# Performance work log

Measured on AMD Instinct MI355X. Metric: run time of the kernel, lower is better.

The kernel has to match this reference:

```python
import jax, jax.numpy as jnp
import numpy as np

M_POS = 0.5
M_NEG_SIM = 0.1
LAM_NEG = 1.0


def setup_inputs() -> dict:
    key = jax.random.key(0)
    N, d, G = 8192, 1024, 64
    codebook = jax.random.normal(key, (N, d), dtype=jnp.float32)
    base = (jnp.arange(N) // G) * G  # contiguous groups of size G (vq_to_range)
    starts = base.astype(jnp.int32)
    ends = (base + G - 1).astype(jnp.int32)
    return {"codebook": codebook, "starts": starts, "ends": ends, "max_i": N - 1}


def reference(codebook, starts, ends, max_i):
    N, d = codebook.shape
    M = min(N, int(max_i) + 1)  # rows processed by the python loop

    # cosine similarity rows [0:M] vs all N
    zn = codebook / jnp.linalg.norm(codebook, axis=-1, keepdims=True)
    cos = jnp.einsum('md,nd->mn', zn[:M], zn)  # (M, N)

    # pairwise Euclidean distances rows [0:M] vs all N via ||a-b||^2 = |a|^2+|b|^2-2ab
    sq = jnp.sum(codebook * codebook, axis=-1)  # (N,)
    dot = jnp.einsum('md,nd->mn', codebook[:M], codebook)  # (M, N)
    d2 = jnp.maximum(sq[:M, None] + sq[None, :] - 2.0 * dot, 0.0)

    j = jnp.arange(N)[None, :]
    i = jnp.arange(M)[:, None]
    in_range = (j >= starts[:M, None]) & (j <= ends[:M, None])
    pos_mask = in_range & (j != i)
    # original: group_mask[i]=False then neg = ~group_mask, so i is in negatives
    neg_mask = (~in_range) | (j == i)

    pos_cnt = jnp.sum(pos_mask, axis=-1)
    neg_cnt = jnp.sum(neg_mask, axis=-1)

    # safe sqrt: only evaluate on positive-mask entries
    D = jnp.sqrt(jnp.where(pos_mask, d2, 1.0))
    pos_term = jnp.square(jax.nn.relu(D - M_POS)) * pos_mask
    pos_pull = jnp.sum(pos_term, axis=-1) / jnp.maximum(pos_cnt, 1)

    neg_cos = jnp.clip(cos, -1.0, 1.0)
    neg_term = jnp.square(jax.nn.relu(jnp.abs(neg_cos) - M_NEG_SIM)) * neg_mask
    ortho = jnp.sum(neg_term, axis=-1) / jnp.maximum(neg_cnt, 1)

    valid = (pos_cnt > 0) & (neg_cnt > 0)
    per_row = jnp.where(valid, pos_pull + LAM_NEG * ortho, 0.0)
    cnt = jnp.sum(valid)
    total = jnp.sum(per_row)
    return jnp.where(cnt > 0, total / jnp.maximum(cnt, 1).astype(total.dtype), jnp.zeros((), total.dtype))
```

## Files before the change

kernel.cpp:

```cpp
#include <hip/hip_runtime.h>
#include <hip/hip_bf16.h>
#include <stdint.h>

#define M_POS 0.5f
#define M_NEG 0.1f
#define LAM_NEG 1.0f

typedef __attribute__((ext_vector_type(4))) float floatx4;
typedef __attribute__((ext_vector_type(8))) int   intx8;

union Frag8 { intx8 v; int4 q[2]; };


__global__ __launch_bounds__(256) void prep_kernel(
    const float* __restrict__ cb, unsigned char* __restrict__ cb_q,
    float* __restrict__ sq, float* __restrict__ inv_norm,
    unsigned* __restrict__ zero_base, int zero_len,
    int N, int d)
{
    const int gi = blockIdx.x * 256 + threadIdx.x;
    if (gi < zero_len) zero_base[gi] = 0u;

    const int row = blockIdx.x;
    const float* src = cb + (size_t)row * d;
    const int t = threadIdx.x;
    const size_t fragRowBase = ((size_t)(row >> 4) * 8) << 11;
    const int rl = row & 15;

    float s = 0.f;
    for (int c = t * 4; c < d; c += 1024) {
        float4 v = *(const float4*)(src + c);
        s += v.x * v.x + v.y * v.y + v.z * v.z + v.w * v.w;
        int pk = __builtin_amdgcn_cvt_pk_fp8_f32(v.x, v.y, 0, false);
        pk     = __builtin_amdgcn_cvt_pk_fp8_f32(v.z, v.w, pk, true);
        const int K = c >> 7;
        const int g = (c >> 5) & 3;
        const int h = (c >> 4) & 1;
        unsigned char* dq = cb_q + fragRowBase + ((size_t)K << 11)
                          + (h << 10) + ((g * 16 + rl) << 4) + (c & 15);
        *(int*)dq = pk;
    }
    for (int o = 32; o > 0; o >>= 1) s += __shfl_down(s, o, 64);
    __shared__ float wsum[4];
    if ((t & 63) == 0) wsum[t >> 6] = s;
    __syncthreads();
    if (t == 0) {
        float tot = wsum[0] + wsum[1] + wsum[2] + wsum[3];
        sq[row] = tot;
        inv_norm[row] = rsqrtf(tot);
    }
}

__global__ __launch_bounds__(256, 2) void gram_loss_kernel(
    const unsigned char* __restrict__ A,
    const float* __restrict__ sq, const float* __restrict__ inv_norm,
    const int* __restrict__ starts, const int* __restrict__ ends,
    const int* __restrict__ max_ip,
    float* __restrict__ pos_acc, float* __restrict__ neg_acc,
    unsigned* __restrict__ counter, float* __restrict__ out,
    int N, int d)
{
    const int M = min(N, max_ip[0] + 1);

    int vt = blockIdx.x;
    const int nB = gridDim.x;
    if ((nB & 7) == 0) {
        const int per = nB >> 3;
        vt = (blockIdx.x & 7) * per + (blockIdx.x >> 3);
    }

    int bx = (int)((sqrtf(8.f * (float)vt + 1.f) - 1.f) * 0.5f);
    while ((bx + 1) * (bx + 2) / 2 <= vt) bx++;
    while (bx * (bx + 1) / 2 > vt) bx--;
    const int by = vt - bx * (bx + 1) / 2;

    const int rowBase = by * 128;
    const int colBase = bx * 128;
    const bool isDiag = (by == bx);

    const int tid  = threadIdx.x;
    const int wave = tid >> 6;
    const int lane = tid & 63;
    const int wr = (wave >> 1) * 64;
    const int wc = (wave & 1) * 64;

    floatx4 acc[4][4];
#pragma unroll
    for (int a = 0; a < 4; ++a)
#pragma unroll
        for (int b = 0; b < 4; ++b) acc[a][b] = (floatx4){0.f, 0.f, 0.f, 0.f};

    const int kTiles = d / 128;
    const int rl = lane & 15;

    const unsigned char* aBase = A + ((((size_t)((rowBase + wr) >> 4)) * 8) << 11) + (lane << 4);
    const unsigned char* bBase = A + ((((size_t)((colBase + wc) >> 4)) * 8) << 11) + (lane << 4);

    Frag8 aX[4], bX[4], aY[4], bY[4];

#define LOADF(AF, BF, KT)                                                    \
    { _Pragma("unroll")                                                      \
      for (int t4 = 0; t4 < 4; ++t4) {                                       \
        const size_t off_ = ((size_t)(t4 * 8 + (KT))) << 11;                 \
        AF[t4].q[0] = *(const int4*)(aBase + off_);                          \
        AF[t4].q[1] = *(const int4*)(aBase + off_ + 1024);                   \
        BF[t4].q[0] = *(const int4*)(bBase + off_);                          \
        BF[t4].q[1] = *(const int4*)(bBase + off_ + 1024);                   \
      } }

#define MFMAS(AF, BF)                                                        \
    { _Pragma("unroll")                                                      \
      for (int rt = 0; rt < 4; ++rt)                                         \
        _Pragma("unroll")                                                    \
        for (int ct = 0; ct < 4; ++ct)                                       \
          acc[rt][ct] = __builtin_amdgcn_mfma_scale_f32_16x16x128_f8f6f4(    \
              AF[rt].v, BF[ct].v, acc[rt][ct], 0, 0, 0, 127, 0, 127); }

    LOADF(aX, bX, 0)
    int kt = 0;
    for (;;) {
        if (kt + 1 < kTiles) LOADF(aY, bY, kt + 1)
        __builtin_amdgcn_sched_barrier(0);
        MFMAS(aX, bX)
        ++kt; if (kt >= kTiles) break;
        if (kt + 1 < kTiles) LOADF(aX, bX, kt + 1)
        __builtin_amdgcn_sched_barrier(0);
        MFMAS(aY, bY)
        ++kt; if (kt >= kTiles) break;
    }
#undef LOADF
#undef MFMAS

    const int q  = lane >> 4;
    const int jlo = colBase + wc;
    const int ilo = rowBase + wr;

    int   jn[4];
    float jinv[4];
    bool  jvalid[4];
#pragma unroll
    for (int ct = 0; ct < 4; ++ct) {
        const int j = jlo + ct * 16 + rl;
        jn[ct]  = j;
        jinv[ct] = inv_norm[j];
        jvalid[ct] = (j < M);
    }

    bool posLane = false;
    {
        const int ri = ilo + lane;
        if (ri < M) posLane |= (ends[ri] >= jlo) && (starts[ri] <= jlo + 63);
        if (!isDiag) {
            const int cj = jlo + lane;
            if (cj < M) posLane |= (ends[cj] >= ilo) && (starts[cj] <= ilo + 63);
        }
    }
    const bool fullPath = (__ballot(posLane) != 0ULL);

    float posc[4] = {0.f, 0.f, 0.f, 0.f};
    float negc[4] = {0.f, 0.f, 0.f, 0.f};

    if (fullPath) {
        int   jns[4], jne[4];
        float jsq[4];
#pragma unroll
        for (int ct = 0; ct < 4; ++ct) {
            jsq[ct] = sq[jn[ct]];
            jns[ct] = jvalid[ct] ? starts[jn[ct]] : 0;
            jne[ct] = jvalid[ct] ? ends[jn[ct]]   : -1;
        }
#pragma unroll
        for (int rt = 0; rt < 4; ++rt) {
            const int ibase = ilo + rt * 16 + q * 4;
#pragma unroll
            for (int reg = 0; reg < 4; ++reg) {
                const int i = ibase + reg;
                const bool rowValid = (i < M);
                const int ns = rowValid ? starts[i] : 0;
                const int ne = rowValid ? ends[i]   : -1;
                const float iinv = inv_norm[i];
                const float isq  = sq[i];
                float posp = 0.f, negp = 0.f;
#pragma unroll
                for (int ct = 0; ct < 4; ++ct) {
                    const float dot = acc[rt][ct][reg];
                    const int j = jn[ct];
                    float cosv = dot * iinv * jinv[ct];
                    cosv = fminf(fmaxf(cosv, -1.f), 1.f);
                    float tn = fmaxf(fabsf(cosv) - M_NEG, 0.f);
                    const float nterm = tn * tn;
                    const float d2 = fmaxf(isq + jsq[ct] - 2.f * dot, 0.f);
                    float tp = fmaxf(sqrtf(d2) - M_POS, 0.f);
                    const float pterm = tp * tp;
                    const bool dg = (j == i);
                    if (rowValid) {
                        const bool in_r = (j >= ns) && (j <= ne);
                        if (in_r && !dg) posp += pterm;
                        if (!in_r || dg) negp += nterm;
                    }
                    if (!isDiag && jvalid[ct]) {
                        const bool in_c = (i >= jns[ct]) && (i <= jne[ct]);
                        if (in_c && !dg) posc[ct] += pterm;
                        if (!in_c || dg) negc[ct] += nterm;
                    }
                }
#pragma unroll
                for (int m = 1; m < 16; m <<= 1) {
                    posp += __shfl_xor(posp, m, 64);
                    negp += __shfl_xor(negp, m, 64);
                }
                if (rowValid && rl == 0) {
                    atomicAdd(&pos_acc[i], posp);
                    atomicAdd(&neg_acc[i], negp);
                }
            }
        }
        if (!isDiag) {
#pragma unroll
            for (int ct = 0; ct < 4; ++ct) {
                posc[ct] += __shfl_xor(posc[ct], 16, 64);
                posc[ct] += __shfl_xor(posc[ct], 32, 64);
                negc[ct] += __shfl_xor(negc[ct], 16, 64);
                negc[ct] += __shfl_xor(negc[ct], 32, 64);
            }
            if (q == 0) {
#pragma unroll
                for (int ct = 0; ct < 4; ++ct) {
                    if (jvalid[ct]) {
                        atomicAdd(&pos_acc[jn[ct]], posc[ct]);
                        atomicAdd(&neg_acc[jn[ct]], negc[ct]);
                    }
                }
            }
        }
    } else {
#pragma unroll
        for (int rt = 0; rt < 4; ++rt) {
            const int ibase = ilo + rt * 16 + q * 4;
#pragma unroll
            for (int reg = 0; reg < 4; ++reg) {
                const int i = ibase + reg;
                const float iinv = inv_norm[i];
                float negp = 0.f;
#pragma unroll
                for (int ct = 0; ct < 4; ++ct) {
                    const float dot = acc[rt][ct][reg];
                    float cosv = dot * iinv * jinv[ct];
                    cosv = fminf(fmaxf(cosv, -1.f), 1.f);
                    float tn = fmaxf(fabsf(cosv) - M_NEG, 0.f);
                    const float nterm = tn * tn;
                    negp += nterm;
                    negc[ct] += nterm;
                }
#pragma unroll
                for (int m = 1; m < 16; m <<= 1)
                    negp += __shfl_xor(negp, m, 64);
                if ((i < M) && rl == 0)
                    atomicAdd(&neg_acc[i], negp);
            }
        }
        if (!isDiag) {
#pragma unroll
            for (int ct = 0; ct < 4; ++ct) {
                negc[ct] += __shfl_xor(negc[ct], 16, 64);
                negc[ct] += __shfl_xor(negc[ct], 32, 64);
            }
            if (q == 0) {
#pragma unroll
                for (int ct = 0; ct < 4; ++ct)
                    if (jvalid[ct])
                        atomicAdd(&neg_acc[jn[ct]], negc[ct]);
            }
        }
    }

    __shared__ bool amLast;
    __syncthreads();
    if (tid == 0) {
        __threadfence();
        unsigned old = atomicAdd(counter, 1u);
        amLast = (old == (unsigned)(gridDim.x - 1));
    }
    __syncthreads();
    if (amLast) {
        __threadfence();
        float total = 0.f;
        int cnt = 0;
        for (int i = tid; i < M; i += 256) {
            const float pa = __hip_atomic_load(&pos_acc[i], __ATOMIC_RELAXED, __HIP_MEMORY_SCOPE_AGENT);
            const float na = __hip_atomic_load(&neg_acc[i], __ATOMIC_RELAXED, __HIP_MEMORY_SCOPE_AGENT);
            const int ns = starts[i], ne = ends[i];
            const int lo = max(ns, 0), hi = min(ne, N - 1);
            const int inr = max(hi - lo + 1, 0);
            const bool dg = (i >= ns) && (i <= ne);
            const int pos_cnt = inr - (dg ? 1 : 0);
            const int neg_cnt = N - inr + (dg ? 1 : 0);
            if (pos_cnt > 0 && neg_cnt > 0) {
                total += pa / (float)max(pos_cnt, 1)
                       + LAM_NEG * na / (float)max(neg_cnt, 1);
                cnt++;
            }
        }
        for (int o = 32; o > 0; o >>= 1) {
            total += __shfl_down(total, o, 64);
            cnt   += __shfl_down(cnt, o, 64);
        }
        __shared__ float fin_ts[4];
        __shared__ int   fin_cs[4];
        if ((tid & 63) == 0) { fin_ts[tid >> 6] = total; fin_cs[tid >> 6] = cnt; }
        __syncthreads();
        if (tid == 0) {
            float T = fin_ts[0] + fin_ts[1] + fin_ts[2] + fin_ts[3];
            int   C = fin_cs[0] + fin_cs[1] + fin_cs[2] + fin_cs[3];
            out[0] = (C > 0) ? T / (float)C : 0.f;
        }
    }
}

extern "C" void kernel_launch(void* const* d_in, const int* in_sizes, int n_in,
                              void* d_out, int out_size, void* d_ws, size_t ws_size,
                              hipStream_t stream) {
    const float* cb     = (const float*)d_in[0];
    const int*   starts = (const int*)d_in[1];
    const int*   ends   = (const int*)d_in[2];
    const int*   max_ip = (const int*)d_in[3];
    float* out = (float*)d_out;

    const int N = in_sizes[1];
    const int d = in_sizes[0] / N;

    char* ws = (char*)d_ws;
    unsigned char* cb_q = (unsigned char*)ws;
    size_t off = ((size_t)N * d + 255) & ~(size_t)255;
    float* sq       = (float*)(ws + off); off += (size_t)N * 4;
    float* inv_norm = (float*)(ws + off); off += (size_t)N * 4;
    float* pos_acc  = (float*)(ws + off); off += (size_t)N * 4;
    float* neg_acc  = (float*)(ws + off); off += (size_t)N * 4;
    unsigned* counter = (unsigned*)(ws + off); off += 256;

    prep_kernel<<<N, 256, 0, stream>>>(cb, cb_q, sq, inv_norm,
                                       (unsigned*)pos_acc, 2 * N + 1, N, d);

    const int nb = N / 128;
    const int nBlocks = nb * (nb + 1) / 2;
    gram_loss_kernel<<<nBlocks, 256, 0, stream>>>(cb_q, sq, inv_norm, starts, ends,
                                                  max_ip, pos_acc, neg_acc, counter,
                                                  out, N, d);
}
```

Before: 230.0 us.

## Hand-schedule GEMM fragment loads with asm waitcnt and use one wave per prep row

The fp8 GEMM main loop now issues its fragment loads as inline-asm global_load_dwordx4. An explicit s_waitcnt vmcnt(16) waits only for the previous tile's loads, so the next tile's 16 loads stay in flight while MFMAs run. Without this, the compiler could insert a full vmcnt(0) and serialize loads with compute. The prep kernel now assigns one wave per row with 16-byte packed fp8 stores and drops the shared-memory reduction, and it launches a quarter as many blocks. Fragment addressing now uses kTiles instead of a hardcoded 8. Manual waitcnt handling is fragile: the compiler no longer tracks these loads, so any miscount would read registers before the data arrives.

New measurement: 225.5 us. 2.0% less time.

```diff
diff --git a/kernel.cpp b/kernel.cpp
--- a/kernel.cpp
+++ b/kernel.cpp
@@ -8,8 +8,9 @@
 
 typedef __attribute__((ext_vector_type(4))) float floatx4;
 typedef __attribute__((ext_vector_type(8))) int   intx8;
-
-union Frag8 { intx8 v; int4 q[2]; };
+typedef __attribute__((ext_vector_type(4))) int   int32x4;
+
+union Frag8 { intx8 v; int32x4 q[2]; };
 
 
 __global__ __launch_bounds__(256) void prep_kernel(
@@ -21,34 +22,39 @@
     const int gi = blockIdx.x * 256 + threadIdx.x;
     if (gi < zero_len) zero_base[gi] = 0u;
 
-    const int row = blockIdx.x;
+    const int t = threadIdx.x;
+    const int w = t >> 6, l = t & 63;
+    const int row = blockIdx.x * 4 + w;
+    if (row >= N) return;
+    const int kTiles = d >> 7;
     const float* src = cb + (size_t)row * d;
-    const int t = threadIdx.x;
-    const size_t fragRowBase = ((size_t)(row >> 4) * 8) << 11;
+    unsigned char* fragRow = cb_q + (((size_t)(row >> 4) * kTiles) << 11);
     const int rl = row & 15;
 
     float s = 0.f;
-    for (int c = t * 4; c < d; c += 1024) {
-        float4 v = *(const float4*)(src + c);
-        s += v.x * v.x + v.y * v.y + v.z * v.z + v.w * v.w;
-        int pk = __builtin_amdgcn_cvt_pk_fp8_f32(v.x, v.y, 0, false);
-        pk     = __builtin_amdgcn_cvt_pk_fp8_f32(v.z, v.w, pk, true);
-        const int K = c >> 7;
-        const int g = (c >> 5) & 3;
-        const int h = (c >> 4) & 1;
-        unsigned char* dq = cb_q + fragRowBase + ((size_t)K << 11)
-                          + (h << 10) + ((g * 16 + rl) << 4) + (c & 15);
-        *(int*)dq = pk;
+    for (int c = l * 16; c < d; c += 1024) {
+        float4 v0 = *(const float4*)(src + c);
+        float4 v1 = *(const float4*)(src + c + 4);
+        float4 v2 = *(const float4*)(src + c + 8);
+        float4 v3 = *(const float4*)(src + c + 12);
+        s += v0.x*v0.x + v0.y*v0.y + v0.z*v0.z + v0.w*v0.w
+           + v1.x*v1.x + v1.y*v1.y + v1.z*v1.z + v1.w*v1.w
+           + v2.x*v2.x + v2.y*v2.y + v2.z*v2.z + v2.w*v2.w
+           + v3.x*v3.x + v3.y*v3.y + v3.z*v3.z + v3.w*v3.w;
+        int p0 = __builtin_amdgcn_cvt_pk_fp8_f32(v0.x, v0.y, 0, false);
+        p0     = __builtin_amdgcn_cvt_pk_fp8_f32(v0.z, v0.w, p0, true);
+        int p1 = __builtin_amdgcn_cvt_pk_fp8_f32(v1.x, v1.y, 0, false);
+        p1     = __builtin_amdgcn_cvt_pk_fp8_f32(v1.z, v1.w, p1, true);
+        int p2 = __builtin_amdgcn_cvt_pk_fp8_f32(v2.x, v2.y, 0, false);
+        p2     = __builtin_amdgcn_cvt_pk_fp8_f32(v2.z, v2.w, p2, true);
+        int p3 = __builtin_amdgcn_cvt_pk_fp8_f32(v3.x, v3.y, 0, false);
+        p3     = __builtin_amdgcn_cvt_pk_fp8_f32(v3.z, v3.w, p3, true);
+        int32x4 pk; pk.x = p0; pk.y = p1; pk.z = p2; pk.w = p3;
+        const int K = c >> 7, g = (c >> 5) & 3, h = (c >> 4) & 1;
+        *(int32x4*)(fragRow + ((size_t)K << 11) + (h << 10) + ((g * 16 + rl) << 4)) = pk;
     }
     for (int o = 32; o > 0; o >>= 1) s += __shfl_down(s, o, 64);
-    __shared__ float wsum[4];
-    if ((t & 63) == 0) wsum[t >> 6] = s;
-    __syncthreads();
-    if (t == 0) {
-        float tot = wsum[0] + wsum[1] + wsum[2] + wsum[3];
-        sq[row] = tot;
-        inv_norm[row] = rsqrtf(tot);
-    }
+    if (l == 0) { sq[row] = s; inv_norm[row] = rsqrtf(s); }
 }
 
 __global__ __launch_bounds__(256, 2) void gram_loss_kernel(
@@ -93,43 +99,64 @@
     const int kTiles = d / 128;
     const int rl = lane & 15;
 
-    const unsigned char* aBase = A + ((((size_t)((rowBase + wr) >> 4)) * 8) << 11) + (lane << 4);
-    const unsigned char* bBase = A + ((((size_t)((colBase + wc) >> 4)) * 8) << 11) + (lane << 4);
+    const unsigned char* aBase = A + ((((size_t)((rowBase + wr) >> 4)) * kTiles) << 11) + (lane << 4);
+    const unsigned char* bBase = A + ((((size_t)((colBase + wc) >> 4)) * kTiles) << 11) + (lane << 4);
 
     Frag8 aX[4], bX[4], aY[4], bY[4];
 
-#define LOADF(AF, BF, KT)                                                    \
-    { _Pragma("unroll")                                                      \
-      for (int t4 = 0; t4 < 4; ++t4) {                                       \
-        const size_t off_ = ((size_t)(t4 * 8 + (KT))) << 11;                 \
-        AF[t4].q[0] = *(const int4*)(aBase + off_);                          \
-        AF[t4].q[1] = *(const int4*)(aBase + off_ + 1024);                   \
-        BF[t4].q[0] = *(const int4*)(bBase + off_);                          \
-        BF[t4].q[1] = *(const int4*)(bBase + off_ + 1024);                   \
+#define GL0(dst, p)  asm volatile("global_load_dwordx4 %0, %1, off"             : "=v"(dst) : "v"(p))
+#define GL1(dst, p)  asm volatile("global_load_dwordx4 %0, %1, off offset:1024" : "=v"(dst) : "v"(p))
+
+#define ISSUE(AF, BF, KT)                                                        \
+    { _Pragma("unroll")                                                          \
+      for (int t4 = 0; t4 < 4; ++t4) {                                           \
+        const unsigned char* pa_ = aBase + (((size_t)(t4 * kTiles + (KT))) << 11); \
+        const unsigned char* pb_ = bBase + (((size_t)(t4 * kTiles + (KT))) << 11); \
+        GL0(AF[t4].q[0], pa_); GL1(AF[t4].q[1], pa_);                            \
+        GL0(BF[t4].q[0], pb_); GL1(BF[t4].q[1], pb_);                            \
       } }
 
-#define MFMAS(AF, BF)                                                        \
-    { _Pragma("unroll")                                                      \
-      for (int rt = 0; rt < 4; ++rt)                                         \
-        _Pragma("unroll")                                                    \
-        for (int ct = 0; ct < 4; ++ct)                                       \
-          acc[rt][ct] = __builtin_amdgcn_mfma_scale_f32_16x16x128_f8f6f4(    \
+#define MFMAS(AF, BF)                                                            \
+    { _Pragma("unroll")                                                          \
+      for (int rt = 0; rt < 4; ++rt)                                             \
+        _Pragma("unroll")                                                        \
+        for (int ct = 0; ct < 4; ++ct)                                           \
+          acc[rt][ct] = __builtin_amdgcn_mfma_scale_f32_16x16x128_f8f6f4(        \
               AF[rt].v, BF[ct].v, acc[rt][ct], 0, 0, 0, 127, 0, 127); }
 
-    LOADF(aX, bX, 0)
+    ISSUE(aX, bX, 0)
     int kt = 0;
     for (;;) {
-        if (kt + 1 < kTiles) LOADF(aY, bY, kt + 1)
+        if (kt + 1 < kTiles) {
+            ISSUE(aY, bY, kt + 1)
+            __builtin_amdgcn_sched_barrier(0);
+            asm volatile("s_waitcnt vmcnt(16)");
+        } else {
+            __builtin_amdgcn_sched_barrier(0);
+            asm volatile("s_waitcnt vmcnt(0)");
+        }
         __builtin_amdgcn_sched_barrier(0);
         MFMAS(aX, bX)
+        __builtin_amdgcn_sched_barrier(0);
         ++kt; if (kt >= kTiles) break;
-        if (kt + 1 < kTiles) LOADF(aX, bX, kt + 1)
+
+        if (kt + 1 < kTiles) {
+            ISSUE(aX, bX, kt + 1)
+            __builtin_amdgcn_sched_barrier(0);
+            asm volatile("s_waitcnt vmcnt(16)");
+        } else {
+            __builtin_amdgcn_sched_barrier(0);
+            asm volatile("s_waitcnt vmcnt(0)");
+        }
         __builtin_amdgcn_sched_barrier(0);
         MFMAS(aY, bY)
+        __builtin_amdgcn_sched_barrier(0);
         ++kt; if (kt >= kTiles) break;
     }
-#undef LOADF
+#undef ISSUE
 #undef MFMAS
+#undef GL0
+#undef GL1
 
     const int q  = lane >> 4;
     const int jlo = colBase + wc;
@@ -338,8 +365,8 @@
     float* neg_acc  = (float*)(ws + off); off += (size_t)N * 4;
     unsigned* counter = (unsigned*)(ws + off); off += 256;
 
-    prep_kernel<<<N, 256, 0, stream>>>(cb, cb_q, sq, inv_norm,
-                                       (unsigned*)pos_acc, 2 * N + 1, N, d);
+    prep_kernel<<<(N + 3) / 4, 256, 0, stream>>>(cb, cb_q, sq, inv_norm,
+                                                 (unsigned*)pos_acc, 2 * N + 1, N, d);
 
     const int nb = N / 128;
     const int nBlocks = nb * (nb + 1) / 2;
```
